# Kernel optimization log

Measured on AMD Instinct MI355X. Metric: run time of the kernel, lower is better.

## Reference

```python
import jax, jax.numpy as jnp
import numpy as np

N, C, H, K = 50000, 256, 8, 16
M = N * K
HID = 4 * C
HD = C // H
SCALE = HD ** -0.5
EPS = 1e-5


def setup_inputs() -> dict:
    key = jax.random.key(0)
    ks = jax.random.split(key, 8)
    init = lambda k, shape, fan: jax.random.normal(k, shape, jnp.float32) * (fan ** -0.5)
    return {
        "feats": jax.random.normal(ks[0], (N, C), jnp.float32),
        "polar_pos": jax.random.normal(ks[1], (N, 3), jnp.float32),
        "edge_index": jax.random.randint(ks[2], (2, M), 0, N, dtype=jnp.int64),
        "ln1_g": jnp.ones((C,), jnp.float32), "ln1_b": jnp.zeros((C,), jnp.float32),
        "qkv_w": init(ks[3], (3 * C, C), C), "qkv_b": jnp.zeros((3 * C,), jnp.float32),
        "proj_w": init(ks[4], (C, C), C), "proj_b": jnp.zeros((C,), jnp.float32),
        "ln2_g": jnp.ones((C,), jnp.float32), "ln2_b": jnp.zeros((C,), jnp.float32),
        "fc1_w": init(ks[5], (HID, C), C), "fc1_b": jnp.zeros((HID,), jnp.float32),
        "fc2_w": init(ks[6], (C, HID), HID), "fc2_b": jnp.zeros((C,), jnp.float32),
    }


def _ln(x, g, b):
    m = x.mean(-1, keepdims=True)
    v = jnp.var(x, axis=-1, keepdims=True)
    return (x - m) * jax.lax.rsqrt(v + EPS) * g + b


def reference(feats, polar_pos, edge_index, ln1_g, ln1_b, qkv_w, qkv_b,
              proj_w, proj_b, ln2_g, ln2_b, fc1_w, fc1_b, fc2_w, fc2_b):
    skip = feats
    x = _ln(feats, ln1_g, ln1_b)

    # edge bookkeeping: sort edges by destination (index_0), matching torch.sort
    idx0 = edge_index[0]
    idx1 = edge_index[1]
    order = jnp.argsort(idx0)  # stable sort
    idx0 = idx0[order]
    idx1 = idx1[order]

    # qkv projection -> (N, 3, H, HD)
    qkv = (x @ qkv_w.T + qkv_b).reshape(N, 3, H, HD)
    q = qkv[:, 0] * SCALE  # (N, H, HD)
    k = qkv[:, 1]
    v = qkv[:, 2]

    # attention_step1_v2: per-edge dot products, (M, H)
    attn = jnp.einsum('mhd,mhd->mh', q[idx0], k[idx1])

    # scatter_softmax over edges grouped by idx0
    mx = jax.ops.segment_max(attn, idx0, num_segments=N)
    e = jnp.exp(attn - mx[idx0])
    s = jax.ops.segment_sum(e, idx0, num_segments=N)
    w = e / s[idx0]  # (M, H)

    # attention_step2: weighted aggregation of neighbor values
    out = jax.ops.segment_sum(w[:, :, None] * v[idx1], idx0, num_segments=N)
    out = out.reshape(N, C)

    out = out @ proj_w.T + proj_b
    feats = skip + out

    y = _ln(feats, ln2_g, ln2_b)
    y = jax.nn.gelu(y @ fc1_w.T + fc1_b, approximate=False)
    y = y @ fc2_w.T + fc2_b
    return feats + y
```

## Files before the change

kernel.cpp:

```cpp
#include <hip/hip_runtime.h>
#include <hip/hip_bf16.h>
#include <cmath>


#define N_NODES 50000
#define C_DIM 256
#define M_EDGES 800000
#define ATT_SCALE 0.17677669529663687f
#define LN_EPS 1e-5f
#define LOG2E 1.4426950408889634f
#define NEG_BIG -3.0e38f

typedef unsigned int uint_t;
typedef unsigned short ushort_t;
typedef short short8 __attribute__((ext_vector_type(8)));
typedef float floatx4 __attribute__((ext_vector_type(4)));

__device__ __forceinline__ ushort_t f2bf(float f) {
  uint_t u = __float_as_uint(f);
  return (ushort_t)((u + 0x7FFFu + ((u >> 16) & 1u)) >> 16);
}
__device__ __forceinline__ float bf_even(uint_t u) { return __uint_as_float(u << 16); }
__device__ __forceinline__ float bf_odd(uint_t u) { return __uint_as_float(u & 0xFFFF0000u); }

__device__ __forceinline__ float gelu_tanh(float x) {
  const float u = 0.7978845608028654f * (x + 0.044715f * x * x * x);
  const float e = __expf(2.0f * u);
  const float t = 1.0f - 2.0f / (e + 1.0f);
  return 0.5f * x * (1.0f + t);
}

__device__ __forceinline__ void gload16(const void* g, void* l) {
  __builtin_amdgcn_global_load_lds(
      (const __attribute__((address_space(1))) void*)g,
      (__attribute__((address_space(3))) void*)l, 16, 0, 0);
}

__global__ __launch_bounds__(256) void ln_kernel(const float* __restrict__ x,
    const float* __restrict__ g, const float* __restrict__ b,
    ushort_t* __restrict__ y)
{
  const int row = blockIdx.x * 4 + (threadIdx.x >> 6);
  const int lane = threadIdx.x & 63;
  const float4 v = *(const float4*)(x + (size_t)row * C_DIM + lane * 4);
  float s = v.x + v.y + v.z + v.w;
  float s2 = v.x * v.x + v.y * v.y + v.z * v.z + v.w * v.w;
#pragma unroll
  for (int m = 1; m < 64; m <<= 1) {
    s += __shfl_xor(s, m);
    s2 += __shfl_xor(s2, m);
  }
  const float mean = s * (1.0f / 256.0f);
  const float var = fmaxf(s2 * (1.0f / 256.0f) - mean * mean, 0.0f);
  const float r = rsqrtf(var + LN_EPS);
  const float4 g4 = *(const float4*)(g + lane * 4);
  const float4 b4 = *(const float4*)(b + lane * 4);
  ushort4 o;
  o.x = f2bf((v.x - mean) * r * g4.x + b4.x);
  o.y = f2bf((v.y - mean) * r * g4.y + b4.y);
  o.z = f2bf((v.z - mean) * r * g4.z + b4.z);
  o.w = f2bf((v.w - mean) * r * g4.w + b4.w);
  *(ushort4*)(y + (size_t)row * C_DIM + lane * 4) = o;
}

__global__ void cvt_kernel(const float* __restrict__ s0, const float* __restrict__ s1,
                           const float* __restrict__ s2, const float* __restrict__ s3,
                           ushort_t* __restrict__ dst)
{
  const int i = blockIdx.x * 256 + threadIdx.x;
  float v;
  if (i < 196608) v = s0[i];
  else if (i < 262144) v = s1[i - 196608];
  else if (i < 524288) v = s2[i - 262144];
  else v = s3[i - 524288];
  dst[i] = f2bf(v);
}

template <int EPI>
__global__ __launch_bounds__(256, 3) void mfma_gemm(
    const ushort_t* __restrict__ A, const ushort_t* __restrict__ W,
    const float* __restrict__ bias, const float* __restrict__ extra,
    void* __restrict__ OutV, int Kdim, int Jdim)
{
  __shared__ __align__(16) char smem[40960];
  ushort_t* As = (ushort_t*)smem;
  ushort_t* Bs = As + 64 * 64;
  const int t = threadIdx.x;
  const int lane = t & 63;
  const int w = t >> 6;
  const int wm = w & 1;
  const int wn = w >> 1;
  const int rowbase = blockIdx.y * 64;
  const int colbase = blockIdx.x * 256;

  floatx4 acc[2][8] = {};

  const int base = w * 64 + lane;
  const int rbase = base >> 3;
  const int kcs = (base & 7) ^ (rbase & 7);

  const int rl = lane & 15;
  const int qd = lane >> 4;

  for (int k0 = 0; k0 < Kdim; k0 += 64) {
#pragma unroll
    for (int h = 0; h < 2; ++h) {
      int grow = rowbase + h * 32 + rbase;
      if (grow > N_NODES - 1) grow = N_NODES - 1;
      gload16(A + (size_t)grow * Kdim + k0 + kcs * 8,
              As + (h * 256 + w * 64) * 8);
    }
#pragma unroll
    for (int h = 0; h < 8; ++h) {
      const int gcol = colbase + h * 32 + rbase;
      gload16(W + (size_t)gcol * Kdim + k0 + kcs * 8,
              Bs + (h * 256 + w * 64) * 8);
    }
    __syncthreads();

#pragma unroll
    for (int h = 0; h < 2; ++h) {
      short8 af[2], bf[8];
#pragma unroll
      for (int tm = 0; tm < 2; ++tm) {
        const int ra = wm * 32 + tm * 16 + rl;
        const int kc = (h * 4 + qd) ^ (ra & 7);
        af[tm] = *(const short8*)(As + ra * 64 + kc * 8);
      }
#pragma unroll
      for (int tn = 0; tn < 8; ++tn) {
        const int rb = wn * 128 + tn * 16 + rl;
        const int kc = (h * 4 + qd) ^ (rb & 7);
        bf[tn] = *(const short8*)(Bs + rb * 64 + kc * 8);
      }
#pragma unroll
      for (int tm = 0; tm < 2; ++tm)
#pragma unroll
        for (int tn = 0; tn < 8; ++tn)
          acc[tm][tn] = __builtin_amdgcn_mfma_f32_16x16x32_bf16(
              af[tm], bf[tn], acc[tm][tn], 0, 0, 0);
    }
    __syncthreads();
  }

  const int rr = lane >> 4;
  if (EPI == 1) {
    float* sc = (float*)smem + w * (32 * 68);
    const int c4 = (lane & 15) * 4;
#pragma unroll
    for (int p = 0; p < 2; ++p) {
      __syncthreads();
#pragma unroll
      for (int th = 0; th < 4; ++th) {
        const int tn = p * 4 + th;
#pragma unroll
        for (int tm = 0; tm < 2; ++tm)
#pragma unroll
          for (int r = 0; r < 4; ++r)
            sc[(tm * 16 + qd * 4 + r) * 68 + th * 16 + rl] = acc[tm][tn][r];
      }
      __syncthreads();
      const int col0 = colbase + wn * 128 + p * 64 + c4;
      const float4 b4 = *(const float4*)(bias + col0);
#pragma unroll
      for (int it = 0; it < 8; ++it) {
        const int lr = it * 4 + rr;
        const int grow = rowbase + wm * 32 + lr;
        if (grow >= N_NODES) continue;
        float4 v = *(const float4*)(sc + lr * 68 + c4);
        const float4 e4 = *(const float4*)(extra + (size_t)grow * Jdim + col0);
        v.x += b4.x + e4.x; v.y += b4.y + e4.y;
        v.z += b4.z + e4.z; v.w += b4.w + e4.w;
        *(float4*)((float*)OutV + (size_t)grow * Jdim + col0) = v;
      }
    }
  } else {
    __syncthreads();
    ushort_t* su = (ushort_t*)smem + w * (32 * 136);
#pragma unroll
    for (int tn = 0; tn < 8; ++tn) {
      const int col = colbase + wn * 128 + tn * 16 + rl;
      const float bv = bias[col];
#pragma unroll
      for (int tm = 0; tm < 2; ++tm)
#pragma unroll
        for (int r = 0; r < 4; ++r) {
          float v = acc[tm][tn][r] + bv;
          if (EPI == 0) {
            if (col < 256) v *= ATT_SCALE;
          } else {
            v = gelu_tanh(v);
          }
          su[(tm * 16 + qd * 4 + r) * 136 + tn * 16 + rl] = f2bf(v);
        }
    }
    __syncthreads();
    const int c8 = (lane & 15) * 8;
#pragma unroll
    for (int it = 0; it < 8; ++it) {
      const int lr = it * 4 + rr;
      const int grow = rowbase + wm * 32 + lr;
      if (grow >= N_NODES) continue;
      const uint4 v = *(const uint4*)(su + lr * 136 + c8);
      *(uint4*)((ushort_t*)OutV + (size_t)grow * Jdim + colbase + wn * 128 + c8) = v;
    }
  }
}

__global__ void hist_kernel(const int* __restrict__ idx0, int* __restrict__ counts)
{
  const int m = blockIdx.x * 256 + threadIdx.x;
  if (m < M_EDGES) atomicAdd(&counts[idx0[m]], 1);
}

__global__ __launch_bounds__(256) void scan1_kernel(const int* __restrict__ counts,
    int* __restrict__ offsets, int* __restrict__ bsums)
{
  __shared__ int tmp[256];
  const int t = threadIdx.x;
  const int i = blockIdx.x * 256 + t;
  const int v = (i < N_NODES) ? counts[i] : 0;
  int x = v;
  tmp[t] = x;
  __syncthreads();
#pragma unroll
  for (int off = 1; off < 256; off <<= 1) {
    const int a = (t >= off) ? tmp[t - off] : 0;
    __syncthreads();
    x += a;
    tmp[t] = x;
    __syncthreads();
  }
  if (i < N_NODES) offsets[i] = x - v;
  if (t == 255) bsums[blockIdx.x] = x;
}

__global__ __launch_bounds__(256) void scan2_kernel(int* __restrict__ bsums, int nb)
{
  __shared__ int tmp[256];
  const int t = threadIdx.x;
  const int v = (t < nb) ? bsums[t] : 0;
  int x = v;
  tmp[t] = x;
  __syncthreads();
#pragma unroll
  for (int off = 1; off < 256; off <<= 1) {
    const int a = (t >= off) ? tmp[t - off] : 0;
    __syncthreads();
    x += a;
    tmp[t] = x;
    __syncthreads();
  }
  if (t < nb) bsums[t] = x - v;
}

__global__ void scan3_kernel(int* __restrict__ offsets, const int* __restrict__ bsums)
{
  const int i = blockIdx.x * 256 + threadIdx.x;
  if (i < N_NODES) offsets[i] += bsums[blockIdx.x];
  if (i == 0) offsets[N_NODES] = M_EDGES;
}

__global__ void scatter_kernel(const int* __restrict__ idx0,
    const int* __restrict__ idx1, const int* __restrict__ offsets,
    int* __restrict__ cursor, int* __restrict__ srcs)
{
  const int m = blockIdx.x * 256 + threadIdx.x;
  if (m < M_EDGES) {
    const int n = idx0[m];
    const int p = offsets[n] + atomicAdd(&cursor[n], 1);
    srcs[p] = idx1[m];
  }
}

__global__ __launch_bounds__(256) void attn_kernel(
    const ushort_t* __restrict__ QKVh, const int* __restrict__ offsets,
    const int* __restrict__ srcs, ushort_t* __restrict__ AO)
{
  const int node = blockIdx.x * 4 + (threadIdx.x >> 6);
  if (node >= N_NODES) return;
  const int lane = threadIdx.x & 63;
  const int l32 = lane & 31;
  const int half = lane >> 5;
  const int start = offsets[node];
  const int end = offsets[node + 1];

  const uint4 qp = *(const uint4*)((const uint_t*)(QKVh + (size_t)node * 768) + l32 * 4);

  float m = NEG_BIG, s = 0.f;
  float o[8];
#pragma unroll
  for (int j = 0; j < 8; ++j) o[j] = 0.f;

  for (int e = start + half; e < end; e += 4) {
    const int eB = e + 2;
    const bool hasB = eB < end;
    const int sA = srcs[e];
    const int sB = srcs[hasB ? eB : e];
    const uint_t* rA = (const uint_t*)(QKVh + (size_t)sA * 768);
    const uint_t* rB = (const uint_t*)(QKVh + (size_t)sB * 768);
    const uint4 kA = *(const uint4*)(rA + 128 + l32 * 4);
    const uint4 kB = *(const uint4*)(rB + 128 + l32 * 4);
    const uint4 vA = *(const uint4*)(rA + 256 + l32 * 4);
    const uint4 vB = *(const uint4*)(rB + 256 + l32 * 4);

    float dA = bf_even(qp.x) * bf_even(kA.x) + bf_odd(qp.x) * bf_odd(kA.x)
             + bf_even(qp.y) * bf_even(kA.y) + bf_odd(qp.y) * bf_odd(kA.y)
             + bf_even(qp.z) * bf_even(kA.z) + bf_odd(qp.z) * bf_odd(kA.z)
             + bf_even(qp.w) * bf_even(kA.w) + bf_odd(qp.w) * bf_odd(kA.w);
    dA += __shfl_xor(dA, 1);
    dA += __shfl_xor(dA, 2);
    float dB = bf_even(qp.x) * bf_even(kB.x) + bf_odd(qp.x) * bf_odd(kB.x)
             + bf_even(qp.y) * bf_even(kB.y) + bf_odd(qp.y) * bf_odd(kB.y)
             + bf_even(qp.z) * bf_even(kB.z) + bf_odd(qp.z) * bf_odd(kB.z)
             + bf_even(qp.w) * bf_even(kB.w) + bf_odd(qp.w) * bf_odd(kB.w);
    dB += __shfl_xor(dB, 1);
    dB += __shfl_xor(dB, 2);

    const float lA = dA * LOG2E;
    const float lB = hasB ? dB * LOG2E : NEG_BIG;
    const float mn = fmaxf(m, fmaxf(lA, lB));
    const float fac = exp2f(m - mn);
    const float wA = exp2f(lA - mn);
    const float wB = hasB ? exp2f(lB - mn) : 0.f;
    m = mn;
    s = s * fac + wA + wB;
    o[0] = o[0] * fac + wA * bf_even(vA.x) + wB * bf_even(vB.x);
    o[1] = o[1] * fac + wA * bf_odd(vA.x)  + wB * bf_odd(vB.x);
    o[2] = o[2] * fac + wA * bf_even(vA.y) + wB * bf_even(vB.y);
    o[3] = o[3] * fac + wA * bf_odd(vA.y)  + wB * bf_odd(vB.y);
    o[4] = o[4] * fac + wA * bf_even(vA.z) + wB * bf_even(vB.z);
    o[5] = o[5] * fac + wA * bf_odd(vA.z)  + wB * bf_odd(vB.z);
    o[6] = o[6] * fac + wA * bf_even(vA.w) + wB * bf_even(vB.w);
    o[7] = o[7] * fac + wA * bf_odd(vA.w)  + wB * bf_odd(vB.w);
  }

  const float mO = __shfl_xor(m, 32);
  const float sO = __shfl_xor(s, 32);
  const float mm = fmaxf(m, mO);
  const float fS = exp2f(m - mm);
  const float fO = exp2f(mO - mm);
  const float st = s * fS + sO * fO;
  float out[8];
#pragma unroll
  for (int j = 0; j < 8; ++j) out[j] = o[j] * fS + __shfl_xor(o[j], 32) * fO;

  const float inv = (end > start) ? 1.0f / st : 0.0f;
  if (lane < 32) {
    uint4 st4;
    st4.x = (uint_t)f2bf(out[0] * inv) | ((uint_t)f2bf(out[1] * inv) << 16);
    st4.y = (uint_t)f2bf(out[2] * inv) | ((uint_t)f2bf(out[3] * inv) << 16);
    st4.z = (uint_t)f2bf(out[4] * inv) | ((uint_t)f2bf(out[5] * inv) << 16);
    st4.w = (uint_t)f2bf(out[6] * inv) | ((uint_t)f2bf(out[7] * inv) << 16);
    *(uint4*)((uint_t*)(AO + (size_t)node * 256) + l32 * 4) = st4;
  }
}

extern "C" void kernel_launch(void* const* d_in, const int* in_sizes, int n_in,
                              void* d_out, int out_size, void* d_ws,
                              size_t ws_size, hipStream_t stream)
{
  const float* feats  = (const float*)d_in[0];
  const int*   edge   = (const int*)d_in[2];
  const float* ln1_g  = (const float*)d_in[3];
  const float* ln1_b  = (const float*)d_in[4];
  const float* qkv_w  = (const float*)d_in[5];
  const float* qkv_b  = (const float*)d_in[6];
  const float* proj_w = (const float*)d_in[7];
  const float* proj_b = (const float*)d_in[8];
  const float* ln2_g  = (const float*)d_in[9];
  const float* ln2_b  = (const float*)d_in[10];
  const float* fc1_w  = (const float*)d_in[11];
  const float* fc1_b  = (const float*)d_in[12];
  const float* fc2_w  = (const float*)d_in[13];
  const float* fc2_b  = (const float*)d_in[14];
  float* out = (float*)d_out;

  ushort_t* Xb   = (ushort_t*)d_ws;
  ushort_t* QKVh = Xb + (size_t)N_NODES * 256;
  ushort_t* AOb  = QKVh + (size_t)N_NODES * 768;
  ushort_t* Hb   = QKVh;
  ushort_t* wb   = AOb + (size_t)N_NODES * 256;
  ushort_t* qkv_wb  = wb;
  ushort_t* proj_wb = qkv_wb + 768 * 256;
  ushort_t* fc1_wb  = proj_wb + 256 * 256;
  ushort_t* fc2_wb  = fc1_wb + 1024 * 256;
  int* counts  = (int*)(fc2_wb + 256 * 1024);
  int* cursor  = counts + N_NODES;
  int* offsets = cursor + N_NODES;
  int* srcs    = offsets + N_NODES + 1;
  int* bsums   = srcs + M_EDGES;
  const size_t required = (size_t)((char*)(bsums + 256) - (char*)d_ws);
  if (ws_size < required) {
    hipMemsetAsync(d_out, 0, (size_t)out_size * sizeof(float), stream);
    return;
  }
  const int* idx0 = edge;
  const int* idx1 = edge + M_EDGES;
  const int rowTiles = (N_NODES + 63) / 64;
  const int scanBlocks = (N_NODES + 255) / 256;

  hipMemsetAsync(counts, 0, 2 * N_NODES * sizeof(int), stream);
  cvt_kernel<<<786432 / 256, 256, 0, stream>>>(qkv_w, proj_w, fc1_w, fc2_w, wb);

  ln_kernel<<<N_NODES / 4, 256, 0, stream>>>(feats, ln1_g, ln1_b, Xb);
  mfma_gemm<0><<<dim3(768 / 256, rowTiles), 256, 0, stream>>>(
      Xb, qkv_wb, qkv_b, nullptr, QKVh, 256, 768);
  hist_kernel<<<(M_EDGES + 255) / 256, 256, 0, stream>>>(idx0, counts);
  scan1_kernel<<<scanBlocks, 256, 0, stream>>>(counts, offsets, bsums);
  scan2_kernel<<<1, 256, 0, stream>>>(bsums, scanBlocks);
  scan3_kernel<<<scanBlocks, 256, 0, stream>>>(offsets, bsums);
  scatter_kernel<<<(M_EDGES + 255) / 256, 256, 0, stream>>>(idx0, idx1, offsets,
                                                            cursor, srcs);
  attn_kernel<<<N_NODES / 4, 256, 0, stream>>>(QKVh, offsets, srcs, AOb);
  mfma_gemm<1><<<dim3(256 / 256, rowTiles), 256, 0, stream>>>(
      AOb, proj_wb, proj_b, feats, out, 256, 256);
  ln_kernel<<<N_NODES / 4, 256, 0, stream>>>(out, ln2_g, ln2_b, Xb);
  mfma_gemm<2><<<dim3(1024 / 256, rowTiles), 256, 0, stream>>>(
      Xb, fc1_wb, fc1_b, nullptr, Hb, 256, 1024);
  mfma_gemm<1><<<dim3(256 / 256, rowTiles), 256, 0, stream>>>(
      Hb, fc2_wb, fc2_b, out, out, 1024, 256);
}
```

Before: 554.6 us.

## Double-buffer shared-memory tiles in MFMA GEMM to overlap loads with compute

Shared memory grows to two stages. The next K-tile of A and W is prefetched into the alternate buffer while MFMAs run on the current one, leaving one barrier per iteration. The aim is to hide global-load latency behind compute. In exchange, the larger LDS footprint forces occupancy down from 3 to 2 blocks per CU, as the launch bounds now reflect.

```diff
diff --git a/kernel.cpp b/kernel.cpp
--- a/kernel.cpp
+++ b/kernel.cpp
@@ -77,14 +77,12 @@
 }
 
 template <int EPI>
-__global__ __launch_bounds__(256, 3) void mfma_gemm(
+__global__ __launch_bounds__(256, 2) void mfma_gemm(
     const ushort_t* __restrict__ A, const ushort_t* __restrict__ W,
     const float* __restrict__ bias, const float* __restrict__ extra,
     void* __restrict__ OutV, int Kdim, int Jdim)
 {
-  __shared__ __align__(16) char smem[40960];
-  ushort_t* As = (ushort_t*)smem;
-  ushort_t* Bs = As + 64 * 64;
+  __shared__ __align__(16) char smem[81920];
   const int t = threadIdx.x;
   const int lane = t & 63;
   const int w = t >> 6;
@@ -102,25 +100,53 @@
   const int rl = lane & 15;
   const int qd = lane >> 4;
 
-  for (int k0 = 0; k0 < Kdim; k0 += 64) {
-#pragma unroll
-    for (int h = 0; h < 2; ++h) {
-      int grow = rowbase + h * 32 + rbase;
-      if (grow > N_NODES - 1) grow = N_NODES - 1;
-      gload16(A + (size_t)grow * Kdim + k0 + kcs * 8,
-              As + (h * 256 + w * 64) * 8);
-    }
+  int growA[2];
+#pragma unroll
+  for (int h = 0; h < 2; ++h) {
+    int grow = rowbase + h * 32 + rbase;
+    if (grow > N_NODES - 1) grow = N_NODES - 1;
+    growA[h] = grow;
+  }
+
+  const int nk = Kdim >> 6;
+
+  {
+    ushort_t* Ab = (ushort_t*)smem;
+    ushort_t* Bb = Ab + 4096;
+#pragma unroll
+    for (int h = 0; h < 2; ++h)
+      gload16(A + (size_t)growA[h] * Kdim + kcs * 8, Ab + (h * 256 + w * 64) * 8);
 #pragma unroll
     for (int h = 0; h < 8; ++h) {
       const int gcol = colbase + h * 32 + rbase;
-      gload16(W + (size_t)gcol * Kdim + k0 + kcs * 8,
-              Bs + (h * 256 + w * 64) * 8);
-    }
-    __syncthreads();
-
+      gload16(W + (size_t)gcol * Kdim + kcs * 8, Bb + (h * 256 + w * 64) * 8);
+    }
+  }
+  __syncthreads();
+
+  for (int kt = 0; kt < nk; ++kt) {
+    const int cur = kt & 1;
+    if (kt + 1 < nk) {
+      const int k0n = (kt + 1) << 6;
+      ushort_t* Ab = (ushort_t*)smem + (cur ^ 1) * 20480;
+      ushort_t* Bb = Ab + 4096;
+#pragma unroll
+      for (int h = 0; h < 2; ++h)
+        gload16(A + (size_t)growA[h] * Kdim + k0n + kcs * 8,
+                Ab + (h * 256 + w * 64) * 8);
+#pragma unroll
+      for (int h = 0; h < 8; ++h) {
+        const int gcol = colbase + h * 32 + rbase;
+        gload16(W + (size_t)gcol * Kdim + k0n + kcs * 8,
+                Bb + (h * 256 + w * 64) * 8);
+      }
+    }
+
+    const ushort_t* As = (const ushort_t*)smem + cur * 20480;
+    const ushort_t* Bs = As + 4096;
 #pragma unroll
     for (int h = 0; h < 2; ++h) {
-      short8 af[2], bf[8];
+      short8 af[2], bfr[8];
 #pragma unroll
       for (int tm = 0; tm < 2; ++tm) {
         const int ra = wm * 32 + tm * 16 + rl;
@@ -131,14 +157,14 @@
       for (int tn = 0; tn < 8; ++tn) {
         const int rb = wn * 128 + tn * 16 + rl;
         const int kc = (h * 4 + qd) ^ (rb & 7);
-        bf[tn] = *(const short8*)(Bs + rb * 64 + kc * 8);
+        bfr[tn] = *(const short8*)(Bs + rb * 64 + kc * 8);
       }
 #pragma unroll
       for (int tm = 0; tm < 2; ++tm)
 #pragma unroll
         for (int tn = 0; tn < 8; ++tn)
           acc[tm][tn] = __builtin_amdgcn_mfma_f32_16x16x32_bf16(
-              af[tm], bf[tn], acc[tm][tn], 0, 0, 0);
+              af[tm], bfr[tn], acc[tm][tn], 0, 0, 0);
     }
     __syncthreads();
   }
```

Result: faster. 538.9 us (-2.8%).

## Double-buffer GEMM LDS tiles with K=32 steps and raise occupancy bound

Applied to the files above, without the earlier changes.

Restructures the MFMA GEMM main loop to use two LDS buffers of K=32 slices, prefetching the next slice while computing the current one, with a single barrier per iteration. The swizzle changes to a 4-way XOR pattern for the narrower tile, and B fragments are loaded one at a time to cut live registers. Launch bounds go from 3 to 4 waves per SIMD to allow more resident blocks. The risks are register spills under the tighter bound and more barrier overhead from halving the K step.

```diff
diff --git a/kernel.cpp b/kernel.cpp
--- a/kernel.cpp
+++ b/kernel.cpp
@@ -77,14 +77,12 @@
 }
 
 template <int EPI>
-__global__ __launch_bounds__(256, 3) void mfma_gemm(
+__global__ __launch_bounds__(256, 4) void mfma_gemm(
     const ushort_t* __restrict__ A, const ushort_t* __restrict__ W,
     const float* __restrict__ bias, const float* __restrict__ extra,
     void* __restrict__ OutV, int Kdim, int Jdim)
 {
   __shared__ __align__(16) char smem[40960];
-  ushort_t* As = (ushort_t*)smem;
-  ushort_t* Bs = As + 64 * 64;
   const int t = threadIdx.x;
   const int lane = t & 63;
   const int w = t >> 6;
@@ -95,50 +93,51 @@
 
   floatx4 acc[2][8] = {};
 
-  const int base = w * 64 + lane;
-  const int rbase = base >> 3;
-  const int kcs = (base & 7) ^ (rbase & 7);
+  const int rt = t >> 2;
+  const int kgo = (((t & 3) ^ (rt & 3))) * 8;
+  int growA = rowbase + rt;
+  if (growA > N_NODES - 1) growA = N_NODES - 1;
 
   const int rl = lane & 15;
   const int qd = lane >> 4;
-
-  for (int k0 = 0; k0 < Kdim; k0 += 64) {
-#pragma unroll
-    for (int h = 0; h < 2; ++h) {
-      int grow = rowbase + h * 32 + rbase;
-      if (grow > N_NODES - 1) grow = N_NODES - 1;
-      gload16(A + (size_t)grow * Kdim + k0 + kcs * 8,
-              As + (h * 256 + w * 64) * 8);
+  const int soff = (qd ^ (rl & 3)) * 8;
+
+  const int nk = Kdim >> 5;
+
+  {
+    ushort_t* Ab = (ushort_t*)smem;
+    ushort_t* Bb = Ab + 2048;
+    gload16(A + (size_t)growA * Kdim + kgo, Ab + t * 8);
+#pragma unroll
+    for (int h = 0; h < 4; ++h)
+      gload16(W + (size_t)(colbase + h * 64 + rt) * Kdim + kgo,
+              Bb + (h * 256 + t) * 8);
+  }
+  __syncthreads();
+
+  for (int kt = 0; kt < nk; ++kt) {
+    const int cur = kt & 1;
+    if (kt + 1 < nk) {
+      const int k0n = (kt + 1) << 5;
+      ushort_t* Ab = (ushort_t*)smem + (cur ^ 1) * 10240;
+      ushort_t* Bb = Ab + 2048;
+      gload16(A + (size_t)growA * Kdim + k0n + kgo, Ab + t * 8);
+#pragma unroll
+      for (int h = 0; h < 4; ++h)
+        gload16(W + (size_t)(colbase + h * 64 + rt) * Kdim + k0n + kgo,
+                Bb + (h * 256 + t) * 8);
     }
-#pragma unroll
-    for (int h = 0; h < 8; ++h) {
-      const int gcol = colbase + h * 32 + rbase;
-      gload16(W + (size_t)gcol * Kdim + k0 + kcs * 8,
-              Bs + (h * 256 + w * 64) * 8);
-    }
-    __syncthreads();
-
-#pragma unroll
-    for (int h = 0; h < 2; ++h) {
-      short8 af[2], bf[8];
-#pragma unroll
-      for (int tm = 0; tm < 2; ++tm) {
-        const int ra = wm * 32 + tm * 16 + rl;
-        const int kc = (h * 4 + qd) ^ (ra & 7);
-        af[tm] = *(const short8*)(As + ra * 64 + kc * 8);
-      }
-#pragma unroll
-      for (int tn = 0; tn < 8; ++tn) {
-        const int rb = wn * 128 + tn * 16 + rl;
-        const int kc = (h * 4 + qd) ^ (rb & 7);
-        bf[tn] = *(const short8*)(Bs + rb * 64 + kc * 8);
-      }
-#pragma unroll
-      for (int tm = 0; tm < 2; ++tm)
-#pragma unroll
-        for (int tn = 0; tn < 8; ++tn)
-          acc[tm][tn] = __builtin_amdgcn_mfma_f32_16x16x32_bf16(
-              af[tm], bf[tn], acc[tm][tn], 0, 0, 0);
+
+    const ushort_t* As = (const ushort_t*)smem + cur * 10240;
+    const ushort_t* Bs = As + 2048;
+    short8 af0 = *(const short8*)(As + (wm * 32 + rl) * 32 + soff);
+    short8 af1 = *(const short8*)(As + (wm * 32 + 16 + rl) * 32 + soff);
+#pragma unroll
+    for (int tn = 0; tn < 8; ++tn) {
+      const short8 bfr =
+          *(const short8*)(Bs + (wn * 128 + tn * 16 + rl) * 32 + soff);
+      acc[0][tn] = __builtin_amdgcn_mfma_f32_16x16x32_bf16(af0, bfr, acc[0][tn], 0, 0, 0);
+      acc[1][tn] = __builtin_amdgcn_mfma_f32_16x16x32_bf16(af1, bfr, acc[1][tn], 0, 0, 0);
     }
     __syncthreads();
   }
```

Result: faster. 525.6 us (-5.2%).
